# Kernel tuning notes

Measured on AMD Instinct MI355X. Metric: run time of the kernel, lower is better.

The kernel has to match this reference:

```python
import math
import jax, jax.numpy as jnp
import numpy as np

DIM = 1536; NH = 12; HD = DIM // NH        # head_dim = 128
F, H, W = 4, 20, 26
S = F * H * W                              # 2080 tokens
BLOCK = 128
SPAD = math.ceil(S / BLOCK) * BLOCK        # 2176
EPS = 1e-6
C = HD // 2
SF, SH, SW = C - 2 * (C // 3), C // 3, C // 3   # 22, 21, 21 rotary bands


def _rope_params(max_len, d, theta=10000.0):
    inv = 1.0 / (theta ** (np.arange(0, d, 2, dtype=np.float64) / d))
    return np.outer(np.arange(max_len), inv)   # [max_len, d//2] angles


def _rope(x, freqs, f, h, w):
    # x: [b, s, n, d] with s == f*h*w; freqs: [1024, d//2] angles
    b, s, n, d = x.shape
    ang = jnp.concatenate([
        jnp.broadcast_to(freqs[:f, :SF][:, None, None, :], (f, h, w, SF)),
        jnp.broadcast_to(freqs[:h, SF:SF + SH][None, :, None, :], (f, h, w, SH)),
        jnp.broadcast_to(freqs[:w, SF + SH:C][None, None, :, :], (f, h, w, SW)),
    ], axis=-1).reshape(s, C)
    cos = jnp.cos(ang)[None, :, None, :]
    sin = jnp.sin(ang)[None, :, None, :]
    xr = x.reshape(b, s, n, C, 2)
    x0, x1 = xr[..., 0], xr[..., 1]          # complex mult (x0+ix1)*(cos+isin)
    out = jnp.stack([x0 * cos - x1 * sin, x0 * sin + x1 * cos], axis=-1)
    return out.reshape(b, s, n, d)


def setup_inputs():
    key = jax.random.key(0)
    ks = jax.random.split(key, 6)
    freqs = jnp.asarray(np.concatenate([
        _rope_params(1024, 2 * SF), _rope_params(1024, 2 * SH), _rope_params(1024, 2 * SW)
    ], axis=1), dtype=jnp.float32)           # [1024, 64]
    lin = lambda k: jax.random.normal(k, (DIM, DIM), jnp.float32) * 0.02
    blk = jnp.arange(SPAD) // BLOCK
    # block-causal (128-token blocks) mask, padding keys (>= S) masked out
    mask = (blk[:, None] >= blk[None, :]) & (jnp.arange(SPAD)[None, :] < S)
    return {
        "x": jax.random.normal(ks[0], (1, S, DIM), jnp.float32),
        "freqs": freqs,
        "wq": lin(ks[1]), "bq": jnp.zeros((DIM,), jnp.float32),
        "wk": lin(ks[2]), "bk": jnp.zeros((DIM,), jnp.float32),
        "wv": lin(ks[3]), "bv": jnp.zeros((DIM,), jnp.float32),
        "wo": lin(ks[4]), "bo": jnp.zeros((DIM,), jnp.float32),
        "gq": jnp.ones((DIM,), jnp.float32),
        "gk": jnp.ones((DIM,), jnp.float32),
        "seq_lens": jnp.array([S], jnp.int32),
        "grid_sizes": jnp.array([[F, H, W]], jnp.int32),
        "mask": mask,
    }


def reference(x, freqs, wq, bq, wk, bk, wv, bv, wo, bo, gq, gk, seq_lens, grid_sizes, mask):
    b, s, _ = x.shape
    n, d = NH, HD
    rms = lambda t, g: (t * jax.lax.rsqrt(jnp.mean(t * t, axis=-1, keepdims=True) + EPS)) * g
    q = rms(x @ wq + bq, gq).reshape(b, s, n, d)
    k = rms(x @ wk + bk, gk).reshape(b, s, n, d)
    v = (x @ wv + bv).reshape(b, s, n, d)
    f, h, w = int(grid_sizes[0, 0]), int(grid_sizes[0, 1]), int(grid_sizes[0, 2])
    sl = int(seq_lens[0])
    if sl > 0 and s == 2 * sl:  # teacher forcing: rope each half independently
        q = jnp.concatenate([_rope(q[:, :sl], freqs, f, h, w), _rope(q[:, sl:], freqs, f, h, w)], axis=1)
        k = jnp.concatenate([_rope(k[:, :sl], freqs, f, h, w), _rope(k[:, sl:], freqs, f, h, w)], axis=1)
    else:
        q = _rope(q, freqs, f, h, w)
        k = _rope(k, freqs, f, h, w)
    pad = SPAD - s
    if pad > 0:
        pz = ((0, 0), (0, pad), (0, 0), (0, 0))
        q, k, v = jnp.pad(q, pz), jnp.pad(k, pz), jnp.pad(v, pz)
    scores = jnp.einsum('bqnd,bknd->bnqk', q, k) / math.sqrt(d)
    scores = jnp.where(mask[None, None], scores, -jnp.inf)
    attn = jax.nn.softmax(scores, axis=-1)
    o = jnp.einsum('bnqk,bknd->bqnd', attn, v)[:, :s].reshape(b, s, n * d)
    return o @ wo + bo
```

## Files before the change

kernel.cpp:

```cpp
#include <hip/hip_runtime.h>

#define DIMM   1536
#define NHEAD  12
#define HD     128
#define SEQ    2080
#define SPADN  2176
#define HWPROD 520
#define SCALE  0.08838834764831845f
#define K2F    0.12751744154f

typedef short short8  __attribute__((ext_vector_type(8)));
typedef float floatx4 __attribute__((ext_vector_type(4)));

__device__ __forceinline__ unsigned short f2bf(float f) {
    union { float f; unsigned u; } v; v.f = f;
    return (unsigned short)((v.u + 0x7fffu + ((v.u >> 16) & 1u)) >> 16);
}
__device__ __forceinline__ float bf2f(unsigned short u) {
    union { unsigned u; float f; } v; v.u = ((unsigned)u) << 16;
    return v.f;
}

__device__ __forceinline__ void gld_lds16(const void* g, void* l) {
    __builtin_amdgcn_global_load_lds(
        (const __attribute__((address_space(1))) unsigned int*)g,
        (__attribute__((address_space(3))) unsigned int*)l, 16, 0, 0);
}

__constant__ int c_base[33] = {0,1,2,3,4,5,6,7,
                               8,10,12,14,16,18,20,22,
                               24,27,30,33,36,39,42,45,
                               48,52,56,60,64,68,72,76,
                               80};
#define SLOTS_PER_HEAD 85

__global__ void k_prep(const float* __restrict__ x,
                       const float* __restrict__ w0, const float* __restrict__ w1,
                       const float* __restrict__ w2, const float* __restrict__ w3,
                       unsigned short* __restrict__ xb,
                       unsigned short* __restrict__ t0, unsigned short* __restrict__ t1,
                       unsigned short* __restrict__ t2, unsigned short* __restrict__ t3) {
    int z = blockIdx.z;
    if (z == 4) {
        int n4 = SEQ * DIMM / 4;
        int idx = (blockIdx.y * 24 + blockIdx.x) * 256 + threadIdx.x;
#pragma unroll
        for (int i = 0; i < 6; i++) {
            int p = idx + i * 147456;
            if (p < n4) {
                float4 v = ((const float4*)x)[p];
                ushort4 o;
                o.x = f2bf(v.x); o.y = f2bf(v.y); o.z = f2bf(v.z); o.w = f2bf(v.w);
                ((ushort4*)xb)[p] = o;
            }
        }
        return;
    }
    const float* in = (z == 0) ? w0 : (z == 1) ? w1 : (z == 2) ? w2 : w3;
    unsigned short* out = (z == 0) ? t0 : (z == 1) ? t1 : (z == 2) ? t2 : t3;
    __shared__ float tile[64][65];
    int tx = threadIdx.x & 63, ty = threadIdx.x >> 6;
    int r0 = blockIdx.x * 64, c0 = blockIdx.y * 64;
#pragma unroll
    for (int i = 0; i < 16; i++)
        tile[i * 4 + ty][tx] = in[(size_t)(r0 + i * 4 + ty) * DIMM + c0 + tx];
    __syncthreads();
#pragma unroll
    for (int i = 0; i < 16; i++) {
        int cc = i * 4 + ty;
        out[(size_t)(c0 + cc) * DIMM + r0 + tx] = f2bf(tile[tx][cc]);
    }
}

__global__ __launch_bounds__(256, 3) void k_gemm(
    const unsigned short* __restrict__ A,
    const unsigned short* __restrict__ B0, const unsigned short* __restrict__ B1,
    const unsigned short* __restrict__ B2,
    const float* __restrict__ bias0, const float* __restrict__ bias1, const float* __restrict__ bias2,
    unsigned short* __restrict__ Qh, unsigned short* __restrict__ Kh,
    unsigned short* __restrict__ Vt,
    int M, int N, int K) {
    const unsigned short* B = B0; const float* bias = bias0;
    if (blockIdx.z == 1) { B = B1; bias = bias1; }
    if (blockIdx.z == 2) { B = B2; bias = bias2; }

    __shared__ unsigned short As[128 * 64];
    __shared__ unsigned short Bs[128 * 64];

    int tid = threadIdx.x;
    int lane = tid & 63, wv = tid >> 6;
    int quad = lane >> 4, l16 = lane & 15;
    int m0 = blockIdx.y * 128, n0 = blockIdx.x * 128;
    int wm = (wv >> 1) * 64, wn = (wv & 1) * 64;
    int sw = l16 & 7;

    int srow_in_blk = lane >> 3;
    int schunk = lane & 7;
    int gchunk = schunk ^ (srow_in_blk & 7);

    floatx4 acc[4][4];
#pragma unroll
    for (int i = 0; i < 4; i++)
#pragma unroll
        for (int j = 0; j < 4; j++) acc[i][j] = (floatx4){0.f, 0.f, 0.f, 0.f};

    for (int k0 = 0; k0 < K; k0 += 64) {
#pragma unroll
        for (int i = 0; i < 4; i++) {
            int blkrow = (wv * 4 + i) * 8;
            int r = blkrow + srow_in_blk;
            int ra = m0 + r; if (ra > M - 1) ra = M - 1;
            gld_lds16(A + (size_t)ra * K + k0 + gchunk * 8, &As[blkrow * 64]);
            gld_lds16(B + (size_t)(n0 + r) * K + k0 + gchunk * 8, &Bs[blkrow * 64]);
        }
        __syncthreads();
#pragma unroll
        for (int kc = 0; kc < 2; kc++) {
            short8 af[4], bfr[4];
#pragma unroll
            for (int t = 0; t < 4; t++) {
                int ca = ((kc * 4 + quad) ^ sw) << 3;
                af[t]  = *(const short8*)&As[(wm + t * 16 + l16) * 64 + ca];
                bfr[t] = *(const short8*)&Bs[(wn + t * 16 + l16) * 64 + ca];
            }
#pragma unroll
            for (int mi = 0; mi < 4; mi++)
#pragma unroll
                for (int ni = 0; ni < 4; ni++)
                    acc[mi][ni] = __builtin_amdgcn_mfma_f32_16x16x32_bf16(af[mi], bfr[ni], acc[mi][ni], 0, 0, 0);
        }
        __syncthreads();
    }
    if (blockIdx.z == 2) {
#pragma unroll
        for (int mi = 0; mi < 4; mi++) {
            int row0 = m0 + wm + mi * 16 + quad * 4;
            if (row0 < M) {
#pragma unroll
                for (int ni = 0; ni < 4; ni++) {
                    int col = n0 + wn + ni * 16 + l16;
                    float b = bias[col];
                    ushort4 o;
                    o.x = f2bf(acc[mi][ni][0] + b);
                    o.y = f2bf(acc[mi][ni][1] + b);
                    o.z = f2bf(acc[mi][ni][2] + b);
                    o.w = f2bf(acc[mi][ni][3] + b);
                    *(ushort4*)(Vt + (size_t)col * SPADN + row0) = o;
                }
            }
        }
    } else {
        unsigned short* O = (blockIdx.z == 0) ? Qh : Kh;
#pragma unroll
        for (int mi = 0; mi < 4; mi++) {
#pragma unroll
            for (int r = 0; r < 4; r++) {
                int row = m0 + wm + mi * 16 + quad * 4 + r;
                if (row < M) {
#pragma unroll
                    for (int ni = 0; ni < 4; ni++) {
                        int col = n0 + wn + ni * 16 + l16;
                        O[(size_t)row * DIMM + col] = f2bf(acc[mi][ni][r] + bias[col]);
                    }
                }
            }
        }
    }
}

__global__ __launch_bounds__(256, 8) void k_gemm64(
    const unsigned short* __restrict__ A, const unsigned short* __restrict__ B,
    const float* __restrict__ bias, float* __restrict__ C, int M, int N, int K) {
    __shared__ unsigned short As[64 * 64];
    __shared__ unsigned short Bs[64 * 64];
    int tid = threadIdx.x;
    int lane = tid & 63, wv = tid >> 6;
    int quad = lane >> 4, l16 = lane & 15;
    int m0 = blockIdx.y * 64, n0 = blockIdx.x * 64;
    int wm = (wv >> 1) * 32, wn = (wv & 1) * 32;

    int srow = lane >> 3;
    int schunk = lane & 7;

    floatx4 acc[2][2];
#pragma unroll
    for (int i = 0; i < 2; i++)
#pragma unroll
        for (int j = 0; j < 2; j++) acc[i][j] = (floatx4){0.f, 0.f, 0.f, 0.f};

    for (int k0 = 0; k0 < K; k0 += 64) {
#pragma unroll
        for (int i = 0; i < 2; i++) {
            int rb = (i * 4 + wv) * 8;
            int r = rb + srow;
            int g = schunk ^ (r & 7);
            int ra = m0 + r; if (ra > M - 1) ra = M - 1;
            gld_lds16(A + (size_t)ra * K + k0 + g * 8, &As[rb * 64]);
            gld_lds16(B + (size_t)(n0 + r) * K + k0 + g * 8, &Bs[rb * 64]);
        }
        __syncthreads();
#pragma unroll
        for (int kc = 0; kc < 2; kc++) {
            short8 af[2], bfr[2];
#pragma unroll
            for (int t = 0; t < 2; t++) {
                int rowa = wm + t * 16 + l16;
                int rowb = wn + t * 16 + l16;
                int c = kc * 4 + quad;
                af[t]  = *(const short8*)&As[rowa * 64 + ((c ^ (rowa & 7)) << 3)];
                bfr[t] = *(const short8*)&Bs[rowb * 64 + ((c ^ (rowb & 7)) << 3)];
            }
#pragma unroll
            for (int mi = 0; mi < 2; mi++)
#pragma unroll
                for (int ni = 0; ni < 2; ni++)
                    acc[mi][ni] = __builtin_amdgcn_mfma_f32_16x16x32_bf16(af[mi], bfr[ni], acc[mi][ni], 0, 0, 0);
        }
        __syncthreads();
    }
#pragma unroll
    for (int mi = 0; mi < 2; mi++) {
#pragma unroll
        for (int r = 0; r < 4; r++) {
            int row = m0 + wm + mi * 16 + quad * 4 + r;
            if (row < M) {
#pragma unroll
                for (int ni = 0; ni < 2; ni++) {
                    int col = n0 + wn + ni * 16 + l16;
                    C[(size_t)row * N + col] = acc[mi][ni][r] + bias[col];
                }
            }
        }
    }
}

__global__ void k_rmsrope(const unsigned short* __restrict__ Qh, const unsigned short* __restrict__ Kh,
                          const float* __restrict__ gq, const float* __restrict__ gk,
                          const float* __restrict__ freqs,
                          unsigned short* __restrict__ Qa, unsigned short* __restrict__ Ka) {
    __shared__ float redq[4], redk[4];
    int s = blockIdx.x;
    int tid = threadIdx.x;
    int lane = tid & 63, wv = tid >> 6;
    const ushort2* qrow = (const ushort2*)(Qh + (size_t)s * DIMM);
    const ushort2* krow = (const ushort2*)(Kh + (size_t)s * DIMM);
    const float2* g2q = (const float2*)gq;
    const float2* g2k = (const float2*)gk;

    float2 qv[3], kv[3];
    float sq = 0.f, sk = 0.f;
#pragma unroll
    for (int j = 0; j < 3; j++) {
        int p = tid + j * 256;
        ushort2 uq = qrow[p], uk = krow[p];
        qv[j].x = bf2f(uq.x); qv[j].y = bf2f(uq.y);
        kv[j].x = bf2f(uk.x); kv[j].y = bf2f(uk.y);
        sq += qv[j].x * qv[j].x + qv[j].y * qv[j].y;
        sk += kv[j].x * kv[j].x + kv[j].y * kv[j].y;
    }
#pragma unroll
    for (int m = 32; m >= 1; m >>= 1) { sq += __shfl_xor(sq, m); sk += __shfl_xor(sk, m); }
    if (lane == 0) { redq[wv] = sq; redk[wv] = sk; }
    __syncthreads();
    float tq = redq[0] + redq[1] + redq[2] + redq[3];
    float tk = redk[0] + redk[1] + redk[2] + redk[3];
    float scq = rsqrtf(tq * (1.f / DIMM) + 1e-6f);
    float sck = rsqrtf(tk * (1.f / DIMM) + 1e-6f);

    int fi = s / HWPROD;
    int rem = s - fi * HWPROD;
    int hi = rem / 26;
    int wi = rem - hi * 26;
#pragma unroll
    for (int j = 0; j < 3; j++) {
        int p = tid + j * 256;
        int c = p & 63;
        int pos = (c < 22) ? fi : ((c < 43) ? hi : wi);
        float ang = freqs[pos * 64 + c];
        float sn, cs;
        __sincosf(ang, &sn, &cs);
        float2 gqa = g2q[p];
        float q0 = qv[j].x * scq * gqa.x, q1 = qv[j].y * scq * gqa.y;
        ushort2 oq; oq.x = f2bf(q0 * cs - q1 * sn); oq.y = f2bf(q0 * sn + q1 * cs);
        float2 gka = g2k[p];
        float kk0 = kv[j].x * sck * gka.x, kk1 = kv[j].y * sck * gka.y;
        ushort2 ok; ok.x = f2bf(kk0 * cs - kk1 * sn); ok.y = f2bf(kk0 * sn + kk1 * cs);
        int h = p >> 6;
        size_t off = ((size_t)h * SPADN + s) * HD + 2 * c;
        *(ushort2*)(Qa + off) = oq;
        *(ushort2*)(Ka + off) = ok;
    }
}

__global__ __launch_bounds__(256, 3) void k_attn1(const unsigned short* __restrict__ Qa,
                                                  const unsigned short* __restrict__ Ka,
                                                  const unsigned short* __restrict__ Vt,
                                                  unsigned short* __restrict__ Opart,
                                                  float* __restrict__ Lpart,
                                                  unsigned short* __restrict__ Ob) {
    int j = blockIdx.x, h = blockIdx.y, z = blockIdx.z;
    int nkb = (j >> 1) * 2 + 2;
    if (nkb > 33) nkb = 33;
    int nc = (nkb + 7) >> 3;
    if (z >= nc) return;
    int kb0 = z * 8;
    int kb1 = kb0 + 8; if (kb1 > nkb) kb1 = nkb;

    __shared__ unsigned short Ks[64 * 128];
    __shared__ unsigned short Vs[128 * 64];
    __shared__ unsigned short Ps[4][16][72];

    int tid = threadIdx.x;
    int lane = tid & 63, wv = tid >> 6;
    int quad = lane >> 4, l16 = lane & 15;
    int qrow0 = j * 64 + wv * 16;

    short8 qf[4];
#pragma unroll
    for (int kc = 0; kc < 4; kc++)
        qf[kc] = *(const short8*)(Qa + ((size_t)h * SPADN + qrow0 + l16) * HD + kc * 32 + quad * 8);

    short8 ones8;
#pragma unroll
    for (int i = 0; i < 8; i++) ones8[i] = (short)0x3F80;

    floatx4 of[8], of9;
#pragma unroll
    for (int ni = 0; ni < 8; ni++) of[ni] = (floatx4){0.f, 0.f, 0.f, 0.f};
    of9 = (floatx4){0.f, 0.f, 0.f, 0.f};

    int krow = lane >> 4;
    int kslot = lane & 15;
    int vrow = lane >> 3;
    int vslot = lane & 7;

    for (int kb = kb0; kb < kb1; kb++) {
        const unsigned short* kbase = Ka + (((size_t)h * SPADN + kb * 64) * HD);
#pragma unroll
        for (int i = 0; i < 4; i++) {
            int rb = i * 4 + wv;
            int r = rb * 4 + krow;
            int g = (kslot & 8) | ((kslot & 7) ^ (r & 7));
            gld_lds16(kbase + r * 128 + g * 8, &Ks[rb * 512]);
        }
#pragma unroll
        for (int i = 0; i < 4; i++) {
            int rb = i * 4 + wv;
            int r = rb * 8 + vrow;
            int g = vslot ^ (r & 7);
            gld_lds16(Vt + ((size_t)h * HD + r) * SPADN + kb * 64 + g * 8, &Vs[rb * 512]);
        }
        __syncthreads();

        floatx4 sa[4];
#pragma unroll
        for (int ni = 0; ni < 4; ni++) sa[ni] = (floatx4){0.f, 0.f, 0.f, 0.f};
#pragma unroll
        for (int kc = 0; kc < 4; kc++) {
            int c = kc * 4 + quad;
            short8 kf[4];
#pragma unroll
            for (int ni = 0; ni < 4; ni++) {
                int row = ni * 16 + l16;
                int slot = (c & 8) | ((c & 7) ^ (row & 7));
                kf[ni] = *(const short8*)&Ks[row * 128 + slot * 8];
            }
#pragma unroll
            for (int ni = 0; ni < 4; ni++)
                sa[ni] = __builtin_amdgcn_mfma_f32_16x16x32_bf16(qf[kc], kf[ni], sa[ni], 0, 0, 0);
        }

        bool maskb = (kb == 32);
#pragma unroll
        for (int r = 0; r < 4; r++) {
#pragma unroll
            for (int ni = 0; ni < 4; ni++) {
                float xv = sa[ni][r] * K2F;
                if (maskb && (kb * 64 + ni * 16 + l16 >= SEQ)) xv = -1e30f;
                float p = exp2f(fminf(xv, 36.f));
                Ps[wv][quad * 4 + r][ni * 16 + l16] = f2bf(p);
            }
        }
#pragma unroll
        for (int kc = 0; kc < 2; kc++) {
            int ko = kc * 32 + quad * 8;
            int c = kc * 4 + quad;
            short8 pf = *(const short8*)&Ps[wv][l16][ko];
#pragma unroll
            for (int ni = 0; ni < 8; ni++) {
                int row = ni * 16 + l16;
                short8 vf = *(const short8*)&Vs[row * 64 + ((c ^ (row & 7)) << 3)];
                of[ni] = __builtin_amdgcn_mfma_f32_16x16x32_bf16(pf, vf, of[ni], 0, 0, 0);
            }
            of9 = __builtin_amdgcn_mfma_f32_16x16x32_bf16(pf, ones8, of9, 0, 0, 0);
        }
        __syncthreads();
    }

    if (nc == 1) {
#pragma unroll
        for (int r = 0; r < 4; r++) {
            float inv = 1.f / of9[r];
            int row = qrow0 + quad * 4 + r;
#pragma unroll
            for (int ni = 0; ni < 8; ni++)
                Ob[(size_t)row * DIMM + h * HD + ni * 16 + l16] = f2bf(of[ni][r] * inv);
        }
    } else {
        int slot = h * SLOTS_PER_HEAD + c_base[j] + z;
        unsigned short* Op = Opart + (size_t)slot * 8192;
#pragma unroll
        for (int r = 0; r < 4; r++) {
            int lrow = wv * 16 + quad * 4 + r;
#pragma unroll
            for (int ni = 0; ni < 8; ni++)
                Op[lrow * 128 + ni * 16 + l16] = f2bf(of[ni][r]);
        }
        if (l16 == 0) {
#pragma unroll
            for (int r = 0; r < 4; r++)
                Lpart[slot * 64 + wv * 16 + quad * 4 + r] = of9[r];
        }
    }
}

__global__ void k_attn2(const unsigned short* __restrict__ Opart,
                        const float* __restrict__ Lpart,
                        unsigned short* __restrict__ Ob) {
    int j = blockIdx.x, h = blockIdx.y;
    int nkb = (j >> 1) * 2 + 2; if (nkb > 33) nkb = 33;
    int nc = (nkb + 7) >> 3;
    if (nc == 1) return;
    int base = h * SLOTS_PER_HEAD + c_base[j];
    int t = threadIdx.x;
    int r = t >> 2;
    int c0 = (t & 3) * 32;
    int row = j * 64 + r;
    if (row >= SEQ) return;

    float acc[32];
#pragma unroll
    for (int q = 0; q < 32; q++) acc[q] = 0.f;
    float L = 0.f;
    for (int c = 0; c < nc; c++) {
        int slot = base + c;
        L += Lpart[slot * 64 + r];
        const ushort4* op = (const ushort4*)(Opart + (size_t)slot * 8192 + r * 128 + c0);
#pragma unroll
        for (int q = 0; q < 8; q++) {
            ushort4 u = op[q];
            acc[q * 4 + 0] += bf2f(u.x); acc[q * 4 + 1] += bf2f(u.y);
            acc[q * 4 + 2] += bf2f(u.z); acc[q * 4 + 3] += bf2f(u.w);
        }
    }
    float inv = 1.f / L;
    unsigned short* ob = Ob + (size_t)row * DIMM + h * HD + c0;
#pragma unroll
    for (int q = 0; q < 8; q++) {
        ushort4 o;
        o.x = f2bf(acc[q * 4 + 0] * inv); o.y = f2bf(acc[q * 4 + 1] * inv);
        o.z = f2bf(acc[q * 4 + 2] * inv); o.w = f2bf(acc[q * 4 + 3] * inv);
        *(ushort4*)(ob + q * 4) = o;
    }
}

extern "C" void kernel_launch(void* const* d_in, const int* in_sizes, int n_in,
                              void* d_out, int out_size, void* d_ws, size_t ws_size,
                              hipStream_t stream) {
    const float* x     = (const float*)d_in[0];
    const float* freqs = (const float*)d_in[1];
    const float* wq    = (const float*)d_in[2];
    const float* bq    = (const float*)d_in[3];
    const float* wk    = (const float*)d_in[4];
    const float* bk    = (const float*)d_in[5];
    const float* wv    = (const float*)d_in[6];
    const float* bv    = (const float*)d_in[7];
    const float* wo    = (const float*)d_in[8];
    const float* bo    = (const float*)d_in[9];
    const float* gq    = (const float*)d_in[10];
    const float* gk    = (const float*)d_in[11];
    float* out = (float*)d_out;

    char* ws = (char*)d_ws;
    size_t off = 0;
    auto alloc = [&](size_t bytes) -> void* {
        void* p = ws + off;
        off += (bytes + 255) & ~(size_t)255;
        return p;
    };
    unsigned short* xb  = (unsigned short*)alloc((size_t)SPADN * DIMM * 2);
    unsigned short* wqT = (unsigned short*)alloc((size_t)DIMM * DIMM * 2);
    unsigned short* wkT = (unsigned short*)alloc((size_t)DIMM * DIMM * 2);
    unsigned short* wvT = (unsigned short*)alloc((size_t)DIMM * DIMM * 2);
    unsigned short* Qh  = (unsigned short*)alloc((size_t)SEQ * DIMM * 2);
    unsigned short* Kh  = (unsigned short*)alloc((size_t)SEQ * DIMM * 2);
    unsigned short* woT = (unsigned short*)alloc((size_t)DIMM * DIMM * 2);
    unsigned short* Qa  = (unsigned short*)alloc((size_t)NHEAD * SPADN * HD * 2);
    unsigned short* Ka  = (unsigned short*)alloc((size_t)NHEAD * SPADN * HD * 2);
    unsigned short* Vt  = (unsigned short*)alloc((size_t)DIMM * SPADN * 2);
    unsigned short* Ob  = (unsigned short*)alloc((size_t)SEQ * DIMM * 2);
    float* Lpart = (float*)alloc((size_t)12 * SLOTS_PER_HEAD * 64 * 4);
    unsigned short* Opart = (unsigned short*)ws;
    (void)ws_size; (void)in_sizes; (void)n_in; (void)out_size;

    k_prep<<<dim3(24, 24, 5), 256, 0, stream>>>(x, wq, wk, wv, wo, xb, wqT, wkT, wvT, woT);
    k_gemm<<<dim3(12, 17, 3), 256, 0, stream>>>(xb, wqT, wkT, wvT, bq, bk, bv,
                                                Qh, Kh, Vt, SEQ, DIMM, DIMM);
    k_rmsrope<<<SEQ, 256, 0, stream>>>(Qh, Kh, gq, gk, freqs, Qa, Ka);
    k_attn1<<<dim3(33, 12, 5), 256, 0, stream>>>(Qa, Ka, Vt, Opart, Lpart, Ob);
    k_attn2<<<dim3(33, 12), 256, 0, stream>>>(Opart, Lpart, Ob);
    k_gemm64<<<dim3(24, 33), 256, 0, stream>>>(Ob, woT, bo, out, SEQ, DIMM, DIMM);
}
```

Before: 235.6 us.

## Split attention KV range into 4-block chunks with compact grid

```diff
diff --git a/kernel.cpp b/kernel.cpp
--- a/kernel.cpp
+++ b/kernel.cpp
@@ -27,12 +27,10 @@
         (__attribute__((address_space(3))) unsigned int*)l, 16, 0, 0);
 }
 
-__constant__ int c_base[33] = {0,1,2,3,4,5,6,7,
-                               8,10,12,14,16,18,20,22,
-                               24,27,30,33,36,39,42,45,
-                               48,52,56,60,64,68,72,76,
-                               80};
-#define SLOTS_PER_HEAD 85
+__constant__ int c_base4[34] = {0,1,2,3, 4,6,8,10, 12,15,18,21, 24,28,32,36,
+                                40,45,50,55, 60,66,72,78, 84,91,98,105,
+                                112,120,128,136, 144, 153};
+#define SLOTS_PER_HEAD 153
 
 __global__ void k_prep(const float* __restrict__ x,
                        const float* __restrict__ w0, const float* __restrict__ w1,
@@ -298,13 +296,15 @@
                                                   unsigned short* __restrict__ Opart,
                                                   float* __restrict__ Lpart,
                                                   unsigned short* __restrict__ Ob) {
-    int j = blockIdx.x, h = blockIdx.y, z = blockIdx.z;
+    int s = blockIdx.x, h = blockIdx.y;
+    int j = 0;
+    while (j < 32 && c_base4[j + 1] <= s) j++;
+    int z = s - c_base4[j];
     int nkb = (j >> 1) * 2 + 2;
     if (nkb > 33) nkb = 33;
-    int nc = (nkb + 7) >> 3;
-    if (z >= nc) return;
-    int kb0 = z * 8;
-    int kb1 = kb0 + 8; if (kb1 > nkb) kb1 = nkb;
+    int nc = (nkb + 3) >> 2;
+    int kb0 = z * 4;
+    int kb1 = kb0 + 4; if (kb1 > nkb) kb1 = nkb;
 
     __shared__ unsigned short Ks[64 * 128];
     __shared__ unsigned short Vs[128 * 64];
@@ -370,15 +370,26 @@
                 sa[ni] = __builtin_amdgcn_mfma_f32_16x16x32_bf16(qf[kc], kf[ni], sa[ni], 0, 0, 0);
         }
 
-        bool maskb = (kb == 32);
-#pragma unroll
-        for (int r = 0; r < 4; r++) {
-#pragma unroll
-            for (int ni = 0; ni < 4; ni++) {
-                float xv = sa[ni][r] * K2F;
-                if (maskb && (kb * 64 + ni * 16 + l16 >= SEQ)) xv = -1e30f;
-                float p = exp2f(fminf(xv, 36.f));
-                Ps[wv][quad * 4 + r][ni * 16 + l16] = f2bf(p);
+        if (kb != 32) {
+#pragma unroll
+            for (int r = 0; r < 4; r++) {
+#pragma unroll
+                for (int ni = 0; ni < 4; ni++) {
+                    float p = exp2f(sa[ni][r] * K2F);
+                    Ps[wv][quad * 4 + r][ni * 16 + l16] =
+                        (unsigned short)(__float_as_uint(p) >> 16);
+                }
+            }
+        } else {
+#pragma unroll
+            for (int r = 0; r < 4; r++) {
+#pragma unroll
+                for (int ni = 0; ni < 4; ni++) {
+                    bool pad = (kb * 64 + ni * 16 + l16 >= SEQ);
+                    float p = pad ? 0.f : exp2f(sa[ni][r] * K2F);
+                    Ps[wv][quad * 4 + r][ni * 16 + l16] =
+                        (unsigned short)(__float_as_uint(p) >> 16);
+                }
             }
         }
 #pragma unroll
@@ -407,7 +418,7 @@
                 Ob[(size_t)row * DIMM + h * HD + ni * 16 + l16] = f2bf(of[ni][r] * inv);
         }
     } else {
-        int slot = h * SLOTS_PER_HEAD + c_base[j] + z;
+        int slot = h * SLOTS_PER_HEAD + s;
         unsigned short* Op = Opart + (size_t)slot * 8192;
 #pragma unroll
         for (int r = 0; r < 4; r++) {
@@ -429,9 +440,9 @@
                         unsigned short* __restrict__ Ob) {
     int j = blockIdx.x, h = blockIdx.y;
     int nkb = (j >> 1) * 2 + 2; if (nkb > 33) nkb = 33;
-    int nc = (nkb + 7) >> 3;
+    int nc = (nkb + 3) >> 2;
     if (nc == 1) return;
-    int base = h * SLOTS_PER_HEAD + c_base[j];
+    int base = h * SLOTS_PER_HEAD + c_base4[j];
     int t = threadIdx.x;
     int r = t >> 2;
     int c0 = (t & 3) * 32;
@@ -507,7 +518,7 @@
     k_gemm<<<dim3(12, 17, 3), 256, 0, stream>>>(xb, wqT, wkT, wvT, bq, bk, bv,
                                                 Qh, Kh, Vt, SEQ, DIMM, DIMM);
     k_rmsrope<<<SEQ, 256, 0, stream>>>(Qh, Kh, gq, gk, freqs, Qa, Ka);
-    k_attn1<<<dim3(33, 12, 5), 256, 0, stream>>>(Qa, Ka, Vt, Opart, Lpart, Ob);
+    k_attn1<<<dim3(SLOTS_PER_HEAD, 12), 256, 0, stream>>>(Qa, Ka, Vt, Opart, Lpart, Ob);
     k_attn2<<<dim3(33, 12), 256, 0, stream>>>(Opart, Lpart, Ob);
     k_gemm64<<<dim3(24, 33), 256, 0, stream>>>(Ob, woT, bo, out, SEQ, DIMM, DIMM);
 }
```

Result: slower. 240.8 us (+2.2%).
